# Optimization experiments

Hardware: AMD Instinct MI355X
Metric: run time of the kernel (lower is better)

Reference implementation:

```python
import jax, jax.numpy as jnp
import numpy as np

B = 512      # batch
H = 64       # latent_dim == GRU hidden size
F = 32       # n_features
S = 2048     # seq_len
NEG_SLOPE = 0.01  # nn.LeakyReLU default


def setup_inputs() -> dict:
    key = jax.random.key(0)
    ks = jax.random.split(key, 14)

    def p(k, shape, scale=0.1):
        return jax.random.normal(k, shape, dtype=jnp.float32) * scale

    return {
        "noise": jax.random.normal(ks[0], (B, H), dtype=jnp.float32),
        # GRU forward direction (layer 0): weight_ih_l0, weight_hh_l0, biases
        "W_ih_f": p(ks[1], (3 * H, H)),
        "W_hh_f": p(ks[2], (3 * H, H)),
        "b_ih_f": p(ks[3], (3 * H,)),
        "b_hh_f": p(ks[4], (3 * H,)),
        # GRU backward direction (layer 0 reverse)
        "W_ih_b": p(ks[5], (3 * H, H)),
        "W_hh_b": p(ks[6], (3 * H, H)),
        "b_ih_b": p(ks[7], (3 * H,)),
        "b_hh_b": p(ks[8], (3 * H,)),
        # latent_linear: Linear(2H -> H)
        "W_lat": p(ks[9], (H, 2 * H)),
        "b_lat": p(ks[10], (H,)),
        # output_linear: Linear(H -> F)
        "W_out": p(ks[11], (F, H)),
        "b_out": p(ks[12], (F,)),
    }


def _leaky(x):
    return jnp.where(x >= 0, x, NEG_SLOPE * x)


def _gru_cell(x, h, W_ih, W_hh, b_ih, b_hh):
    # PyTorch GRU cell: gates ordered (r, z, n)
    gi = x @ W_ih.T + b_ih          # (B, 3H)
    gh = h @ W_hh.T + b_hh          # (B, 3H)
    i_r, i_z, i_n = jnp.split(gi, 3, axis=-1)
    h_r, h_z, h_n = jnp.split(gh, 3, axis=-1)
    r = jax.nn.sigmoid(i_r + h_r)
    z = jax.nn.sigmoid(i_z + h_z)
    n = jnp.tanh(i_n + r * h_n)
    return (1.0 - z) * n + z * h


def reference(noise, W_ih_f, W_hh_f, b_ih_f, b_hh_f,
              W_ih_b, W_hh_b, b_ih_b, b_hh_b,
              W_lat, b_lat, W_out, b_out):
    # hidden_state = noise.repeat((D*n_layers,1,1)) -> both directions start at noise
    batch = noise.shape[0]

    def step(carry, _):
        x, hf, hb = carry
        # GRU on a length-1 sequence: each direction does one cell update;
        # output timestep = concat(fwd_out, bwd_out)
        hf2 = _gru_cell(x, hf, W_ih_f, W_hh_f, b_ih_f, b_hh_f)
        hb2 = _gru_cell(x, hb, W_ih_b, W_hh_b, b_ih_b, b_hh_b)
        out = jnp.concatenate([hf2, hb2], axis=-1)        # (B, 2H)
        lat = _leaky(out @ W_lat.T + b_lat)               # (B, H)
        return (lat, hf2, hb2), lat

    x0 = jnp.zeros((batch, H), dtype=noise.dtype)
    _, ys = jax.lax.scan(step, (x0, noise, noise), None, length=S)
    seq = jnp.transpose(ys, (1, 0, 2))   # (B, S, H)
    seq = _leaky(seq)                    # second LeakyReLU as in the original
    out = jax.nn.sigmoid(seq @ W_out.T + b_out)  # (B, S, F)
    return out
```

## Files before the change

kernel.cpp:

```cpp
#include <hip/hip_runtime.h>
#include <hip/hip_bf16.h>


#define NBATCH 512
#define NH 64
#define NS 2048
#define NF 32
#define MROW 16
#define LDH 72

typedef short s16x8 __attribute__((ext_vector_type(8)));
typedef float f32x4 __attribute__((ext_vector_type(4)));

#define MFMA(a, b, c) __builtin_amdgcn_mfma_f32_16x16x32_bf16((a), (b), (c), 0, 0, 0)

#define NLOG2E  (-1.4426950408889634f)
#define N2LOG2E (-2.8853900817779268f)

__device__ __forceinline__ void bar_nodrain() {
    asm volatile("s_barrier" ::: "memory");
}

__device__ __forceinline__ void bar_lgkm() {
    asm volatile("s_waitcnt lgkmcnt(0)\n\ts_barrier" ::: "memory");
}

__device__ __forceinline__ short f2bf(float f) {
    return (short)((__float_as_uint(f) + 0x8000u) >> 16);
}

__device__ __forceinline__ f32x4 v_exp2(f32x4 a) {
    f32x4 r;
#pragma unroll
    for (int i = 0; i < 4; ++i) r[i] = __builtin_amdgcn_exp2f(a[i]);
    return r;
}

__device__ __forceinline__ f32x4 v_rcp(f32x4 a) {
    f32x4 r;
#pragma unroll
    for (int i = 0; i < 4; ++i) r[i] = __builtin_amdgcn_rcpf(a[i]);
    return r;
}

__device__ __forceinline__ f32x4 v_lk(f32x4 a) {
    f32x4 b = a * 0.01f;
    f32x4 r;
#pragma unroll
    for (int i = 0; i < 4; ++i) r[i] = fmaxf(a[i], b[i]);
    return r;
}

__device__ __forceinline__ f32x4 v_lk2(f32x4 a) {
    f32x4 b = a * 1e-4f;
    f32x4 r;
#pragma unroll
    for (int i = 0; i < 4; ++i) r[i] = fmaxf(a[i], b[i]);
    return r;
}

__device__ __forceinline__ f32x4 v_sigm_pre(f32x4 a) {
    return v_rcp(v_exp2(a) + 1.0f);
}

__device__ __forceinline__ int2 pk4bf(f32x4 v) {
    union { __hip_bfloat162 b; int i; } lo, hi;
    float2 a; a.x = v[0]; a.y = v[1];
    float2 b; b.x = v[2]; b.y = v[3];
    lo.b = __float22bfloat162_rn(a);
    hi.b = __float22bfloat162_rn(b);
    int2 r; r.x = lo.i; r.y = hi.i;
    return r;
}

__device__ __forceinline__ s16x8 bfragW(const float* __restrict__ W, int ldk,
                                        int row, int kf, int quad, float scale) {
    const float* p = W + (size_t)row * ldk + kf * 32 + quad * 8;
    s16x8 r;
#pragma unroll
    for (int i = 0; i < 8; ++i) r[i] = f2bf(p[i] * scale);
    return r;
}

__device__ __forceinline__ f32x4 bias4s(const float* __restrict__ p, float scale) {
    const float4 v = *(const float4*)p;
    f32x4 r = {v.x * scale, v.y * scale, v.z * scale, v.w * scale};
    return r;
}

__global__ __launch_bounds__(768)
void grugan_kernel(const float* __restrict__ noise,
                   const float* __restrict__ Wihf, const float* __restrict__ Whhf,
                   const float* __restrict__ bihf, const float* __restrict__ bhhf,
                   const float* __restrict__ Wihb, const float* __restrict__ Whhb,
                   const float* __restrict__ bihb, const float* __restrict__ bhhb,
                   const float* __restrict__ Wlat, const float* __restrict__ blat,
                   const float* __restrict__ Wout, const float* __restrict__ bout,
                   float* __restrict__ out)
{
    __shared__ __align__(16) short Xs[2][MROW][LDH];
    __shared__ __align__(16) short X2s[2][MROW][LDH];
    __shared__ __align__(16) short Hs[2][2][MROW][LDH];

    const int tid  = threadIdx.x;
    const int wave = tid >> 6;
    const int lane = tid & 63;
    const int n    = lane & 15;
    const int quad = lane >> 4;
    const int row0 = blockIdx.x * MROW;

    for (int idx = tid; idx < MROW * LDH; idx += 768) (&Xs[0][0][0])[idx] = 0;
    f32x4 hreg = {0.f, 0.f, 0.f, 0.f};
    const int gdir = wave >> 2;
    const int gjq  = (wave & 3) * 16 + quad * 4;
    if (wave < 8) {
        const float4 nz = *(const float4*)&noise[(size_t)(row0 + n) * NH + gjq];
        hreg[0] = nz.x; hreg[1] = nz.y; hreg[2] = nz.z; hreg[3] = nz.w;
        *(int2*)&Hs[0][gdir][n][gjq] = pk4bf(hreg);
    }
    __syncthreads();

    if (wave < 8) {
        const int dir  = gdir;
        const int cb   = wave & 3;
        const int jrow = cb * 16 + n;
        const int jq   = gjq;
        const float* Wih = dir ? Wihb : Wihf;
        const float* Whh = dir ? Whhb : Whhf;
        const float* bih = dir ? bihb : bihf;
        const float* bhh = dir ? bhhb : bhhf;

        s16x8 wir0 = bfragW(Wih, NH,   0 + jrow, 0, quad, NLOG2E);
        s16x8 wir1 = bfragW(Wih, NH,   0 + jrow, 1, quad, NLOG2E);
        s16x8 wiz0 = bfragW(Wih, NH,  64 + jrow, 0, quad, NLOG2E);
        s16x8 wiz1 = bfragW(Wih, NH,  64 + jrow, 1, quad, NLOG2E);
        s16x8 win0 = bfragW(Wih, NH, 128 + jrow, 0, quad, N2LOG2E);
        s16x8 win1 = bfragW(Wih, NH, 128 + jrow, 1, quad, N2LOG2E);
        s16x8 whr0 = bfragW(Whh, NH,   0 + jrow, 0, quad, NLOG2E);
        s16x8 whr1 = bfragW(Whh, NH,   0 + jrow, 1, quad, NLOG2E);
        s16x8 whz0 = bfragW(Whh, NH,  64 + jrow, 0, quad, NLOG2E);
        s16x8 whz1 = bfragW(Whh, NH,  64 + jrow, 1, quad, NLOG2E);
        s16x8 whn0 = bfragW(Whh, NH, 128 + jrow, 0, quad, N2LOG2E);
        s16x8 whn1 = bfragW(Whh, NH, 128 + jrow, 1, quad, N2LOG2E);
        f32x4 initR, initZ;
        {
            f32x4 a = bias4s(&bih[jq], NLOG2E), b = bias4s(&bhh[jq], NLOG2E);
            initR = a + b;
            f32x4 c = bias4s(&bih[64 + jq], NLOG2E), d = bias4s(&bhh[64 + jq], NLOG2E);
            initZ = c + d;
        }
        const f32x4 initN1 = bias4s(&bih[128 + jq], N2LOG2E);
        const f32x4 initN2 = bias4s(&bhh[128 + jq], N2LOG2E);

        f32x4 accR, accZ, accN2;
        {
            s16x8 ha0 = *(const s16x8*)&Hs[0][dir][n][quad * 8];
            s16x8 ha1 = *(const s16x8*)&Hs[0][dir][n][32 + quad * 8];
            accR  = MFMA(whr0, ha0, initR);  accR  = MFMA(whr1, ha1, accR);
            accZ  = MFMA(whz0, ha0, initZ);  accZ  = MFMA(whz1, ha1, accZ);
            accN2 = MFMA(whn0, ha0, initN2); accN2 = MFMA(whn1, ha1, accN2);
        }

#define GSTEP(HB) do {                                                          \
        __builtin_amdgcn_s_setprio(1);       \
        s16x8 xa0 = *(const s16x8*)&Xs[HB][n][quad * 8];                        \
        s16x8 xa1 = *(const s16x8*)&Xs[HB][n][32 + quad * 8];                   \
        accR = MFMA(wir0, xa0, accR);   accR = MFMA(wir1, xa1, accR);           \
        accZ = MFMA(wiz0, xa0, accZ);   accZ = MFMA(wiz1, xa1, accZ);           \
        f32x4 accN1 = MFMA(win0, xa0, initN1);                                  \
        accN1 = MFMA(win1, xa1, accN1);                                         \
           \
        f32x4 eR = v_exp2(accR);                                                \
        f32x4 rr = v_rcp(eR + 1.0f);                                            \
        f32x4 eU = v_exp2(accN1 + rr * accN2);                                  \
        f32x4 eZ = v_exp2(accZ);                                                \
        f32x4 numer = (eZ + hreg) + eU * (hreg - eZ);                           \
        f32x4 denom = (eU + 1.0f) * (eZ + 1.0f);                                \
        hreg = numer * v_rcp(denom);                                            \
        *(int2*)&Hs[(HB) ^ 1][dir][n][jq] = pk4bf(hreg);                        \
        __builtin_amdgcn_s_setprio(0);         \
        __syncthreads();                                \
        {                                                                       \
            s16x8 ha0 = *(const s16x8*)&Hs[(HB) ^ 1][dir][n][quad * 8];         \
            s16x8 ha1 = *(const s16x8*)&Hs[(HB) ^ 1][dir][n][32 + quad * 8];    \
            accR  = MFMA(whr0, ha0, initR);  accR  = MFMA(whr1, ha1, accR);     \
            accZ  = MFMA(whz0, ha0, initZ);  accZ  = MFMA(whz1, ha1, accZ);     \
            accN2 = MFMA(whn0, ha0, initN2); accN2 = MFMA(whn1, ha1, accN2);    \
        }                                                                       \
        __syncthreads();                                \
    } while (0)

        for (int t = 0; t < NS; t += 2) {
            GSTEP(0);
            GSTEP(1);
        }
#undef GSTEP
    } else {
        const int lt = wave & 3;
        const int nq = lt * 16 + quad * 4;
        s16x8 wl0 = bfragW(Wlat, 2 * NH, lt * 16 + n, 0, quad, 1.0f);
        s16x8 wl1 = bfragW(Wlat, 2 * NH, lt * 16 + n, 1, quad, 1.0f);
        s16x8 wl2 = bfragW(Wlat, 2 * NH, lt * 16 + n, 2, quad, 1.0f);
        s16x8 wl3 = bfragW(Wlat, 2 * NH, lt * 16 + n, 3, quad, 1.0f);
        const f32x4 initL = bias4s(&blat[lt * 16 + quad * 4], 1.0f);

        s16x8 wo0 = {};
        s16x8 wo1 = {};
        f32x4 initO = {0.f, 0.f, 0.f, 0.f};
        float* orow = nullptr;
        if (lt < 2) {
            const int f0 = lt * 16;
            wo0   = bfragW(Wout, NH, f0 + n, 0, quad, NLOG2E);
            wo1   = bfragW(Wout, NH, f0 + n, 1, quad, NLOG2E);
            initO = bias4s(&bout[f0 + quad * 4], NLOG2E);
            orow  = out + (size_t)(row0 + n) * (NS * NF) + f0 + quad * 4;
        }
        const f32x4 zero4 = {0.f, 0.f, 0.f, 0.f};

#define LOSTEP(HB, T) do {                                                      \
        if (lt < 2 && (T) > 0) {                                                \
                  \
                \
            s16x8 p0 = *(const s16x8*)&X2s[HB][n][quad * 8];                    \
            s16x8 p1 = *(const s16x8*)&X2s[HB][n][32 + quad * 8];               \
            f32x4 po = MFMA(wo0, p0, initO);                                    \
            po = MFMA(wo1, p1, po);                                             \
            *(f32x4*)(orow + (size_t)((T) - 1) * NF) = v_sigm_pre(po);          \
        }                                                                       \
        bar_nodrain();        \
        __builtin_amdgcn_s_setprio(1);       \
        s16x8 fa0 = *(const s16x8*)&Hs[(HB) ^ 1][0][n][quad * 8];               \
        s16x8 fa1 = *(const s16x8*)&Hs[(HB) ^ 1][0][n][32 + quad * 8];          \
        s16x8 ba0 = *(const s16x8*)&Hs[(HB) ^ 1][1][n][quad * 8];               \
        s16x8 ba1 = *(const s16x8*)&Hs[(HB) ^ 1][1][n][32 + quad * 8];          \
        f32x4 lac1 = MFMA(wl0, fa0, initL);                                     \
        lac1 = MFMA(wl1, fa1, lac1);                                            \
        f32x4 lac2 = MFMA(wl2, ba0, zero4);                                     \
        lac2 = MFMA(wl3, ba1, lac2);                                            \
        f32x4 la = lac1 + lac2;                                                 \
        *(int2*)&Xs[(HB) ^ 1][n][nq]  = pk4bf(v_lk(la));                        \
        *(int2*)&X2s[(HB) ^ 1][n][nq] = pk4bf(v_lk2(la));                       \
        __builtin_amdgcn_s_setprio(0);           \
        bar_lgkm();                   \
    } while (0)

        for (int t = 0; t < NS; t += 2) {
            LOSTEP(0, t);
            LOSTEP(1, t + 1);
        }
#undef LOSTEP

        if (lt < 2) {
            s16x8 p0 = *(const s16x8*)&X2s[0][n][quad * 8];
            s16x8 p1 = *(const s16x8*)&X2s[0][n][32 + quad * 8];
            f32x4 po = MFMA(wo0, p0, initO);
            po = MFMA(wo1, p1, po);
            *(f32x4*)(orow + (size_t)(NS - 1) * NF) = v_sigm_pre(po);
        }
    }
}

extern "C" void kernel_launch(void* const* d_in, const int* in_sizes, int n_in,
                              void* d_out, int out_size, void* d_ws, size_t ws_size,
                              hipStream_t stream) {
    const float* noise = (const float*)d_in[0];
    const float* Wihf  = (const float*)d_in[1];
    const float* Whhf  = (const float*)d_in[2];
    const float* bihf  = (const float*)d_in[3];
    const float* bhhf  = (const float*)d_in[4];
    const float* Wihb  = (const float*)d_in[5];
    const float* Whhb  = (const float*)d_in[6];
    const float* bihb  = (const float*)d_in[7];
    const float* bhhb  = (const float*)d_in[8];
    const float* Wlat  = (const float*)d_in[9];
    const float* blat  = (const float*)d_in[10];
    const float* Wout  = (const float*)d_in[11];
    const float* bout  = (const float*)d_in[12];

    grugan_kernel<<<dim3(NBATCH / MROW), dim3(768), 0, stream>>>(
        noise, Wihf, Whhf, bihf, bhhf, Wihb, Whhb, bihb, bhhb,
        Wlat, blat, Wout, bout, (float*)d_out);
}
```

Baseline: 1.506 ms.

## Fold latent and output linear work into GRU waves, dropping dedicated waves

```diff
diff --git a/kernel.cpp b/kernel.cpp
--- a/kernel.cpp
+++ b/kernel.cpp
@@ -16,10 +16,6 @@
 
 #define NLOG2E  (-1.4426950408889634f)
 #define N2LOG2E (-2.8853900817779268f)
-
-__device__ __forceinline__ void bar_nodrain() {
-    asm volatile("s_barrier" ::: "memory");
-}
 
 __device__ __forceinline__ void bar_lgkm() {
     asm volatile("s_waitcnt lgkmcnt(0)\n\ts_barrier" ::: "memory");
@@ -88,7 +84,7 @@
     return r;
 }
 
-__global__ __launch_bounds__(768)
+__global__ __launch_bounds__(512)
 void grugan_kernel(const float* __restrict__ noise,
                    const float* __restrict__ Wihf, const float* __restrict__ Whhf,
                    const float* __restrict__ bihf, const float* __restrict__ bhhf,
@@ -109,67 +105,91 @@
     const int quad = lane >> 4;
     const int row0 = blockIdx.x * MROW;
 
-    for (int idx = tid; idx < MROW * LDH; idx += 768) (&Xs[0][0][0])[idx] = 0;
-    f32x4 hreg = {0.f, 0.f, 0.f, 0.f};
-    const int gdir = wave >> 2;
-    const int gjq  = (wave & 3) * 16 + quad * 4;
-    if (wave < 8) {
-        const float4 nz = *(const float4*)&noise[(size_t)(row0 + n) * NH + gjq];
+    const int dir = wave >> 2;
+    const int cb  = wave & 3;
+    const int jq  = cb * 16 + quad * 4;
+
+    for (int idx = tid; idx < MROW * LDH; idx += 512) (&Xs[0][0][0])[idx] = 0;
+    f32x4 hreg;
+    {
+        const float4 nz = *(const float4*)&noise[(size_t)(row0 + n) * NH + jq];
         hreg[0] = nz.x; hreg[1] = nz.y; hreg[2] = nz.z; hreg[3] = nz.w;
-        *(int2*)&Hs[0][gdir][n][gjq] = pk4bf(hreg);
+        *(int2*)&Hs[0][dir][n][jq] = pk4bf(hreg);
     }
     __syncthreads();
 
-    if (wave < 8) {
-        const int dir  = gdir;
-        const int cb   = wave & 3;
-        const int jrow = cb * 16 + n;
-        const int jq   = gjq;
-        const float* Wih = dir ? Wihb : Wihf;
-        const float* Whh = dir ? Whhb : Whhf;
-        const float* bih = dir ? bihb : bihf;
-        const float* bhh = dir ? bhhb : bhhf;
-
-        s16x8 wir0 = bfragW(Wih, NH,   0 + jrow, 0, quad, NLOG2E);
-        s16x8 wir1 = bfragW(Wih, NH,   0 + jrow, 1, quad, NLOG2E);
-        s16x8 wiz0 = bfragW(Wih, NH,  64 + jrow, 0, quad, NLOG2E);
-        s16x8 wiz1 = bfragW(Wih, NH,  64 + jrow, 1, quad, NLOG2E);
-        s16x8 win0 = bfragW(Wih, NH, 128 + jrow, 0, quad, N2LOG2E);
-        s16x8 win1 = bfragW(Wih, NH, 128 + jrow, 1, quad, N2LOG2E);
-        s16x8 whr0 = bfragW(Whh, NH,   0 + jrow, 0, quad, NLOG2E);
-        s16x8 whr1 = bfragW(Whh, NH,   0 + jrow, 1, quad, NLOG2E);
-        s16x8 whz0 = bfragW(Whh, NH,  64 + jrow, 0, quad, NLOG2E);
-        s16x8 whz1 = bfragW(Whh, NH,  64 + jrow, 1, quad, NLOG2E);
-        s16x8 whn0 = bfragW(Whh, NH, 128 + jrow, 0, quad, N2LOG2E);
-        s16x8 whn1 = bfragW(Whh, NH, 128 + jrow, 1, quad, N2LOG2E);
-        f32x4 initR, initZ;
-        {
-            f32x4 a = bias4s(&bih[jq], NLOG2E), b = bias4s(&bhh[jq], NLOG2E);
-            initR = a + b;
-            f32x4 c = bias4s(&bih[64 + jq], NLOG2E), d = bias4s(&bhh[64 + jq], NLOG2E);
-            initZ = c + d;
-        }
-        const f32x4 initN1 = bias4s(&bih[128 + jq], N2LOG2E);
-        const f32x4 initN2 = bias4s(&bhh[128 + jq], N2LOG2E);
-
-        f32x4 accR, accZ, accN2;
-        {
-            s16x8 ha0 = *(const s16x8*)&Hs[0][dir][n][quad * 8];
-            s16x8 ha1 = *(const s16x8*)&Hs[0][dir][n][32 + quad * 8];
-            accR  = MFMA(whr0, ha0, initR);  accR  = MFMA(whr1, ha1, accR);
-            accZ  = MFMA(whz0, ha0, initZ);  accZ  = MFMA(whz1, ha1, accZ);
-            accN2 = MFMA(whn0, ha0, initN2); accN2 = MFMA(whn1, ha1, accN2);
-        }
-
-#define GSTEP(HB) do {                                                          \
-        __builtin_amdgcn_s_setprio(1);       \
+    const int jrow = cb * 16 + n;
+    const float* Wih = dir ? Wihb : Wihf;
+    const float* Whh = dir ? Whhb : Whhf;
+    const float* bih = dir ? bihb : bihf;
+    const float* bhh = dir ? bhhb : bhhf;
+
+    s16x8 wir0 = bfragW(Wih, NH,   0 + jrow, 0, quad, NLOG2E);
+    s16x8 wir1 = bfragW(Wih, NH,   0 + jrow, 1, quad, NLOG2E);
+    s16x8 wiz0 = bfragW(Wih, NH,  64 + jrow, 0, quad, NLOG2E);
+    s16x8 wiz1 = bfragW(Wih, NH,  64 + jrow, 1, quad, NLOG2E);
+    s16x8 win0 = bfragW(Wih, NH, 128 + jrow, 0, quad, N2LOG2E);
+    s16x8 win1 = bfragW(Wih, NH, 128 + jrow, 1, quad, N2LOG2E);
+    s16x8 whr0 = bfragW(Whh, NH,   0 + jrow, 0, quad, NLOG2E);
+    s16x8 whr1 = bfragW(Whh, NH,   0 + jrow, 1, quad, NLOG2E);
+    s16x8 whz0 = bfragW(Whh, NH,  64 + jrow, 0, quad, NLOG2E);
+    s16x8 whz1 = bfragW(Whh, NH,  64 + jrow, 1, quad, NLOG2E);
+    s16x8 whn0 = bfragW(Whh, NH, 128 + jrow, 0, quad, N2LOG2E);
+    s16x8 whn1 = bfragW(Whh, NH, 128 + jrow, 1, quad, N2LOG2E);
+    f32x4 initR, initZ;
+    {
+        f32x4 a = bias4s(&bih[jq], NLOG2E), b = bias4s(&bhh[jq], NLOG2E);
+        initR = a + b;
+        f32x4 c = bias4s(&bih[64 + jq], NLOG2E), d = bias4s(&bhh[64 + jq], NLOG2E);
+        initZ = c + d;
+    }
+    const f32x4 initN1 = bias4s(&bih[128 + jq], N2LOG2E);
+    const f32x4 initN2 = bias4s(&bhh[128 + jq], N2LOG2E);
+
+    s16x8 wl0 = {}, wl1 = {}, wl2 = {}, wl3 = {};
+    f32x4 initL = {0.f, 0.f, 0.f, 0.f};
+    int nq = 0;
+    if (dir == 0) {
+        const int lt = cb;
+        nq  = lt * 16 + quad * 4;
+        wl0 = bfragW(Wlat, 2 * NH, lt * 16 + n, 0, quad, 1.0f);
+        wl1 = bfragW(Wlat, 2 * NH, lt * 16 + n, 1, quad, 1.0f);
+        wl2 = bfragW(Wlat, 2 * NH, lt * 16 + n, 2, quad, 1.0f);
+        wl3 = bfragW(Wlat, 2 * NH, lt * 16 + n, 3, quad, 1.0f);
+        initL = bias4s(&blat[lt * 16 + quad * 4], 1.0f);
+    }
+
+    s16x8 wo0 = {}, wo1 = {};
+    f32x4 initO = {0.f, 0.f, 0.f, 0.f};
+    float* orow = nullptr;
+    const bool outw = (wave == 4) || (wave == 5);
+    if (outw) {
+        const int f0 = cb * 16;
+        wo0   = bfragW(Wout, NH, f0 + n, 0, quad, NLOG2E);
+        wo1   = bfragW(Wout, NH, f0 + n, 1, quad, NLOG2E);
+        initO = bias4s(&bout[f0 + quad * 4], NLOG2E);
+        orow  = out + (size_t)(row0 + n) * (NS * NF) + f0 + quad * 4;
+    }
+    const f32x4 zero4 = {0.f, 0.f, 0.f, 0.f};
+
+    f32x4 accR, accZ, accN2;
+    {
+        s16x8 ha0 = *(const s16x8*)&Hs[0][dir][n][quad * 8];
+        s16x8 ha1 = *(const s16x8*)&Hs[0][dir][n][32 + quad * 8];
+        accR  = MFMA(whr0, ha0, initR);  accR  = MFMA(whr1, ha1, accR);
+        accZ  = MFMA(whz0, ha0, initZ);  accZ  = MFMA(whz1, ha1, accZ);
+        accN2 = MFMA(whn0, ha0, initN2); accN2 = MFMA(whn1, ha1, accN2);
+    }
+
+#define STEP(HB, T) do {                                                        \
+                                    \
+        __builtin_amdgcn_s_setprio(1);                                          \
         s16x8 xa0 = *(const s16x8*)&Xs[HB][n][quad * 8];                        \
         s16x8 xa1 = *(const s16x8*)&Xs[HB][n][32 + quad * 8];                   \
         accR = MFMA(wir0, xa0, accR);   accR = MFMA(wir1, xa1, accR);           \
         accZ = MFMA(wiz0, xa0, accZ);   accZ = MFMA(wiz1, xa1, accZ);           \
         f32x4 accN1 = MFMA(win0, xa0, initN1);                                  \
         accN1 = MFMA(win1, xa1, accN1);                                         \
-           \
         f32x4 eR = v_exp2(accR);                                                \
         f32x4 rr = v_rcp(eR + 1.0f);                                            \
         f32x4 eU = v_exp2(accN1 + rr * accN2);                                  \
@@ -178,85 +198,57 @@
         f32x4 denom = (eU + 1.0f) * (eZ + 1.0f);                                \
         hreg = numer * v_rcp(denom);                                            \
         *(int2*)&Hs[(HB) ^ 1][dir][n][jq] = pk4bf(hreg);                        \
-        __builtin_amdgcn_s_setprio(0);         \
-        __syncthreads();                                \
-        {                                                                       \
-            s16x8 ha0 = *(const s16x8*)&Hs[(HB) ^ 1][dir][n][quad * 8];         \
-            s16x8 ha1 = *(const s16x8*)&Hs[(HB) ^ 1][dir][n][32 + quad * 8];    \
-            accR  = MFMA(whr0, ha0, initR);  accR  = MFMA(whr1, ha1, accR);     \
-            accZ  = MFMA(whz0, ha0, initZ);  accZ  = MFMA(whz1, ha1, accZ);     \
-            accN2 = MFMA(whn0, ha0, initN2); accN2 = MFMA(whn1, ha1, accN2);    \
+        __builtin_amdgcn_s_setprio(0);                                          \
+        bar_lgkm();                                     \
+                                                            \
+        if (dir == 0) {                                                         \
+              \
+            __builtin_amdgcn_s_setprio(1);                                      \
+            s16x8 fa0 = *(const s16x8*)&Hs[(HB) ^ 1][0][n][quad * 8];           \
+            s16x8 fa1 = *(const s16x8*)&Hs[(HB) ^ 1][0][n][32 + quad * 8];      \
+            s16x8 ba0 = *(const s16x8*)&Hs[(HB) ^ 1][1][n][quad * 8];           \
+            s16x8 ba1 = *(const s16x8*)&Hs[(HB) ^ 1][1][n][32 + quad * 8];      \
+            f32x4 lac1 = MFMA(wl0, fa0, initL);                                 \
+            lac1 = MFMA(wl1, fa1, lac1);                                        \
+            f32x4 lac2 = MFMA(wl2, ba0, zero4);                                 \
+            lac2 = MFMA(wl3, ba1, lac2);                                        \
+            f32x4 la = lac1 + lac2;                                             \
+            *(int2*)&Xs[(HB) ^ 1][n][nq]  = pk4bf(v_lk(la));                    \
+            *(int2*)&X2s[(HB) ^ 1][n][nq] = pk4bf(v_lk2(la));                   \
+            accR  = MFMA(whr0, fa0, initR);  accR  = MFMA(whr1, fa1, accR);     \
+            accZ  = MFMA(whz0, fa0, initZ);  accZ  = MFMA(whz1, fa1, accZ);     \
+            accN2 = MFMA(whn0, fa0, initN2); accN2 = MFMA(whn1, fa1, accN2);    \
+            __builtin_amdgcn_s_setprio(0);                                      \
+        } else {                                                                \
+                 \
+            s16x8 ba0 = *(const s16x8*)&Hs[(HB) ^ 1][1][n][quad * 8];           \
+            s16x8 ba1 = *(const s16x8*)&Hs[(HB) ^ 1][1][n][32 + quad * 8];      \
+            accR  = MFMA(whr0, ba0, initR);  accR  = MFMA(whr1, ba1, accR);     \
+            accZ  = MFMA(whz0, ba0, initZ);  accZ  = MFMA(whz1, ba1, accZ);     \
+            accN2 = MFMA(whn0, ba0, initN2); accN2 = MFMA(whn1, ba1, accN2);    \
+            if (outw && (T) > 0) {                                              \
+                s16x8 p0 = *(const s16x8*)&X2s[HB][n][quad * 8];                \
+                s16x8 p1 = *(const s16x8*)&X2s[HB][n][32 + quad * 8];           \
+                f32x4 po = MFMA(wo0, p0, initO);                                \
+                po = MFMA(wo1, p1, po);                                         \
+                *(f32x4*)(orow + (size_t)((T) - 1) * NF) = v_sigm_pre(po);      \
+            }                                                                   \
         }                                                                       \
-        __syncthreads();                                \
+        bar_lgkm();                                     \
     } while (0)
 
-        for (int t = 0; t < NS; t += 2) {
-            GSTEP(0);
-            GSTEP(1);
-        }
-#undef GSTEP
-    } else {
-        const int lt = wave & 3;
-        const int nq = lt * 16 + quad * 4;
-        s16x8 wl0 = bfragW(Wlat, 2 * NH, lt * 16 + n, 0, quad, 1.0f);
-        s16x8 wl1 = bfragW(Wlat, 2 * NH, lt * 16 + n, 1, quad, 1.0f);
-        s16x8 wl2 = bfragW(Wlat, 2 * NH, lt * 16 + n, 2, quad, 1.0f);
-        s16x8 wl3 = bfragW(Wlat, 2 * NH, lt * 16 + n, 3, quad, 1.0f);
-        const f32x4 initL = bias4s(&blat[lt * 16 + quad * 4], 1.0f);
-
-        s16x8 wo0 = {};
-        s16x8 wo1 = {};
-        f32x4 initO = {0.f, 0.f, 0.f, 0.f};
-        float* orow = nullptr;
-        if (lt < 2) {
-            const int f0 = lt * 16;
-            wo0   = bfragW(Wout, NH, f0 + n, 0, quad, NLOG2E);
-            wo1   = bfragW(Wout, NH, f0 + n, 1, quad, NLOG2E);
-            initO = bias4s(&bout[f0 + quad * 4], NLOG2E);
-            orow  = out + (size_t)(row0 + n) * (NS * NF) + f0 + quad * 4;
-        }
-        const f32x4 zero4 = {0.f, 0.f, 0.f, 0.f};
-
-#define LOSTEP(HB, T) do {                                                      \
-        if (lt < 2 && (T) > 0) {                                                \
-                  \
-                \
-            s16x8 p0 = *(const s16x8*)&X2s[HB][n][quad * 8];                    \
-            s16x8 p1 = *(const s16x8*)&X2s[HB][n][32 + quad * 8];               \
-            f32x4 po = MFMA(wo0, p0, initO);                                    \
-            po = MFMA(wo1, p1, po);                                             \
-            *(f32x4*)(orow + (size_t)((T) - 1) * NF) = v_sigm_pre(po);          \
-        }                                                                       \
-        bar_nodrain();        \
-        __builtin_amdgcn_s_setprio(1);       \
-        s16x8 fa0 = *(const s16x8*)&Hs[(HB) ^ 1][0][n][quad * 8];               \
-        s16x8 fa1 = *(const s16x8*)&Hs[(HB) ^ 1][0][n][32 + quad * 8];          \
-        s16x8 ba0 = *(const s16x8*)&Hs[(HB) ^ 1][1][n][quad * 8];               \
-        s16x8 ba1 = *(const s16x8*)&Hs[(HB) ^ 1][1][n][32 + quad * 8];          \
-        f32x4 lac1 = MFMA(wl0, fa0, initL);                                     \
-        lac1 = MFMA(wl1, fa1, lac1);                                            \
-        f32x4 lac2 = MFMA(wl2, ba0, zero4);                                     \
-        lac2 = MFMA(wl3, ba1, lac2);                                            \
-        f32x4 la = lac1 + lac2;                                                 \
-        *(int2*)&Xs[(HB) ^ 1][n][nq]  = pk4bf(v_lk(la));                        \
-        *(int2*)&X2s[(HB) ^ 1][n][nq] = pk4bf(v_lk2(la));                       \
-        __builtin_amdgcn_s_setprio(0);           \
-        bar_lgkm();                   \
-    } while (0)
-
-        for (int t = 0; t < NS; t += 2) {
-            LOSTEP(0, t);
-            LOSTEP(1, t + 1);
-        }
-#undef LOSTEP
-
-        if (lt < 2) {
-            s16x8 p0 = *(const s16x8*)&X2s[0][n][quad * 8];
-            s16x8 p1 = *(const s16x8*)&X2s[0][n][32 + quad * 8];
-            f32x4 po = MFMA(wo0, p0, initO);
-            po = MFMA(wo1, p1, po);
-            *(f32x4*)(orow + (size_t)(NS - 1) * NF) = v_sigm_pre(po);
-        }
+    for (int t = 0; t < NS; t += 2) {
+        STEP(0, t);
+        STEP(1, t + 1);
+    }
+#undef STEP
+
+    if (outw) {
+        s16x8 p0 = *(const s16x8*)&X2s[0][n][quad * 8];
+        s16x8 p1 = *(const s16x8*)&X2s[0][n][32 + quad * 8];
+        f32x4 po = MFMA(wo0, p0, initO);
+        po = MFMA(wo1, p1, po);
+        *(f32x4*)(orow + (size_t)(NS - 1) * NF) = v_sigm_pre(po);
     }
 }
 
@@ -277,7 +269,7 @@
     const float* Wout  = (const float*)d_in[11];
     const float* bout  = (const float*)d_in[12];
 
-    grugan_kernel<<<dim3(NBATCH / MROW), dim3(768), 0, stream>>>(
+    grugan_kernel<<<dim3(NBATCH / MROW), dim3(512), 0, stream>>>(
         noise, Wihf, Whhf, bihf, bhhf, Wihb, Whhb, bihb, bhhb,
         Wlat, blat, Wout, bout, (float*)d_out);
 }
```

After: 1.553 ms. 1.03x slower.
